# Kernel optimization log

Measured on AMD Instinct MI355X. Metric: run time of the kernel, lower is better.

Reference implementation:

```python
import jax, jax.numpy as jnp
import numpy as np

N_NODES = 100000


def setup_inputs() -> dict:
    key = jax.random.key(0)
    k1, k2, k3 = jax.random.split(key, 3)
    x = jax.random.normal(k1, (N_NODES, 64), dtype=jnp.float32)
    edge_index = jax.random.randint(k2, (2, 1250000), 0, N_NODES, dtype=jnp.int64)
    W = jax.random.normal(k3, (128, 64), dtype=jnp.float32) * (1.0 / np.sqrt(128.0))
    b = jnp.zeros((64,), dtype=jnp.float32)
    return {"x": x, "edge_index": edge_index, "W": W, "b": b}


def reference(x, edge_index, W, b):
    n = x.shape[0]
    row, col = edge_index[0], edge_index[1]
    # scatter-add neighbor features onto destination nodes
    neigh = jax.ops.segment_sum(x[row], col, num_segments=n)          # [n, d]
    count = jax.ops.segment_sum(jnp.ones_like(col, dtype=x.dtype), col, num_segments=n)
    count = jnp.where(count == 0, jnp.asarray(1.0, x.dtype), count)   # avoid div-by-zero
    neigh = neigh / count[:, None]                                    # mean aggregation
    x_aggr = jnp.concatenate([x, neigh], axis=-1)                     # [n, 2d]
    out = x_aggr @ W + b                                              # [n, out_dim]
    return jax.nn.relu(out)  # dropout=0.0 (eval) -> identity
```

## Files before the change

### kernel.cpp

```cpp
#include <hip/hip_runtime.h>

#define D 64
#define NPB 64
#define THREADS 512
#define CAP 64

typedef int v4i __attribute__((ext_vector_type(4)));
typedef short bf16x8 __attribute__((ext_vector_type(8)));
typedef float f32x4 __attribute__((ext_vector_type(4)));

__device__ __forceinline__ unsigned short f2bf(float f) {
  unsigned u = __float_as_uint(f);
  return (unsigned short)((u + 0x7FFFu + ((u >> 16) & 1u)) >> 16);
}
__device__ __forceinline__ float bf2f(unsigned short h) {
  return __uint_as_float(((unsigned)h) << 16);
}
__device__ __forceinline__ void bfsplit(float v, unsigned short& hi, unsigned short& lo) {
  unsigned u = __float_as_uint(v);
  hi = (unsigned short)(u >> 16);
  float r = v - __uint_as_float(u & 0xFFFF0000u);
  lo = f2bf(r);
}

__global__ __launch_bounds__(256) void prep0_kernel(
    const float* __restrict__ x, ushort* __restrict__ xh,
    int* __restrict__ cnt, const float* __restrict__ W,
    ushort* __restrict__ wth, ushort* __restrict__ wtl,
    int n, int total4) {
  int t = blockIdx.x * blockDim.x + threadIdx.x;
  int nth = gridDim.x * blockDim.x;
  for (int i = t; i < n; i += nth) cnt[i] = 0;
  for (int i = t; i < 2 * D * D; i += nth) {
    int nn = i >> 7, k = i & 127;
    float v = W[k * D + nn];
    unsigned short hi, lo;
    bfsplit(v, hi, lo);
    wth[i] = hi;
    wtl[i] = lo;
  }
  for (int i = t; i < total4; i += nth) {
    float4 v = ((const float4*)x)[i];
    ushort4 h;
    h.x = f2bf(v.x); h.y = f2bf(v.y); h.z = f2bf(v.z); h.w = f2bf(v.w);
    ((ushort4*)xh)[i] = h;
  }
}

__global__ __launch_bounds__(256) void fill_xcd_kernel(
    const int* __restrict__ ei, int* __restrict__ cnt,
    int* __restrict__ bucket, int e, int qpc) {
  const int myx = blockIdx.x & 7;
  const int chunk = blockIdx.x >> 3;
  const int quads = e >> 2;
  const v4i* row4 = (const v4i*)ei;
  const v4i* col4 = (const v4i*)(ei + e);
  int qend = chunk * qpc + qpc;
  if (qend > quads) qend = quads;
  for (int q = chunk * qpc + threadIdx.x; q < qend; q += 256) {
    v4i r = __builtin_nontemporal_load(&row4[q]);
    v4i c = __builtin_nontemporal_load(&col4[q]);
    if (((c.x >> 11) & 7) == myx) {
      int p = atomicAdd(&cnt[c.x], 1);
      if (p < CAP) bucket[(size_t)c.x * CAP + p] = r.x * D;
    }
    if (((c.y >> 11) & 7) == myx) {
      int p = atomicAdd(&cnt[c.y], 1);
      if (p < CAP) bucket[(size_t)c.y * CAP + p] = r.y * D;
    }
    if (((c.z >> 11) & 7) == myx) {
      int p = atomicAdd(&cnt[c.z], 1);
      if (p < CAP) bucket[(size_t)c.z * CAP + p] = r.z * D;
    }
    if (((c.w >> 11) & 7) == myx) {
      int p = atomicAdd(&cnt[c.w], 1);
      if (p < CAP) bucket[(size_t)c.w * CAP + p] = r.w * D;
    }
  }
}

__global__ __launch_bounds__(THREADS, 8) void fused_bf_kernel(
    const float* __restrict__ x, const ushort* __restrict__ xh,
    const int* __restrict__ cnt,
    const ushort* __restrict__ wth, const ushort* __restrict__ wtl,
    const float* __restrict__ b, float* __restrict__ out, int n) {
  __shared__ __align__(16) ushort xsh[NPB * 128];
  __shared__ __align__(16) ushort xsl[NPB * 128];

  const int lane = threadIdx.x & 63;
  const int wid  = threadIdx.x >> 6;
  const int base = blockIdx.x * NPB;
  const int* bucket = (const int*)out;
  const ushort* xpl = xh + lane;

  for (int m = 0; m < 8; ++m) {
    int nl = wid * 8 + m;
    int node = base + nl;
    int koff = nl * 128;
    int k0 = lane ^ ((nl & 7) << 3);
    if (node < n) {
      int dg = cnt[node];
      int dc = dg < CAP ? dg : CAP;
      int bk = bucket[(size_t)node * CAP + lane];
      float xown = x[(size_t)node * D + lane];
      float s0 = 0.f, s1 = 0.f, s2 = 0.f, s3 = 0.f;
      float s4 = 0.f, s5 = 0.f, s6 = 0.f, s7 = 0.f;
      int p = 0;
      for (; p + 8 <= dc; p += 8) {
        int a0 = __shfl(bk, p),     a1 = __shfl(bk, p + 1);
        int a2 = __shfl(bk, p + 2), a3 = __shfl(bk, p + 3);
        int a4 = __shfl(bk, p + 4), a5 = __shfl(bk, p + 5);
        int a6 = __shfl(bk, p + 6), a7 = __shfl(bk, p + 7);
        s0 += bf2f(xpl[a0]); s1 += bf2f(xpl[a1]);
        s2 += bf2f(xpl[a2]); s3 += bf2f(xpl[a3]);
        s4 += bf2f(xpl[a4]); s5 += bf2f(xpl[a5]);
        s6 += bf2f(xpl[a6]); s7 += bf2f(xpl[a7]);
      }
      for (; p + 4 <= dc; p += 4) {
        int a0 = __shfl(bk, p),     a1 = __shfl(bk, p + 1);
        int a2 = __shfl(bk, p + 2), a3 = __shfl(bk, p + 3);
        s0 += bf2f(xpl[a0]); s1 += bf2f(xpl[a1]);
        s2 += bf2f(xpl[a2]); s3 += bf2f(xpl[a3]);
      }
      for (; p < dc; ++p)
        s0 += bf2f(xpl[__shfl(bk, p)]);
      float sum = ((s0 + s1) + (s2 + s3)) + ((s4 + s5) + (s6 + s7));
      float inv = (dg > 0) ? (1.0f / (float)dg) : 0.0f;
      float mean = sum * inv;
      unsigned short h, l;
      bfsplit(xown, h, l);
      xsh[koff + k0] = h;       xsl[koff + k0] = l;
      bfsplit(mean, h, l);
      xsh[koff + 64 + k0] = h;  xsl[koff + 64 + k0] = l;
    } else {
      xsh[koff + k0] = 0;       xsl[koff + k0] = 0;
      xsh[koff + 64 + k0] = 0;  xsl[koff + 64 + k0] = 0;
    }
  }
  __syncthreads();

  const int mt   = wid >> 1;
  const int nb   = (wid & 1) * 32;
  const int lrow = lane & 15;
  const int kgrp = (lane >> 4) * 8;

  const int arow = mt * 16 + lrow;
  const int aswz = (arow & 7) << 3;
  const int abase = arow * 128;

  const ushort* wh0 = wth + (nb + lrow) * 128;
  const ushort* wh1 = wth + (nb + 16 + lrow) * 128;
  const ushort* wl0 = wtl + (nb + lrow) * 128;
  const ushort* wl1 = wtl + (nb + 16 + lrow) * 128;

  float bias0 = b[nb + lrow];
  float bias1 = b[nb + 16 + lrow];
  f32x4 acc0 = {bias0, bias0, bias0, bias0};
  f32x4 acc1 = {bias1, bias1, bias1, bias1};

#pragma unroll 2
  for (int ks = 0; ks < 4; ++ks) {
    int kb = ks * 32 + kgrp;
    int ke = abase + (kb ^ aswz);
    bf16x8 ah = *(const bf16x8*)&xsh[ke];
    bf16x8 al = *(const bf16x8*)&xsl[ke];
    bf16x8 w0h = *(const bf16x8*)(wh0 + kb);
    bf16x8 w1h = *(const bf16x8*)(wh1 + kb);
    acc0 = __builtin_amdgcn_mfma_f32_16x16x32_bf16(ah, w0h, acc0, 0, 0, 0);
    acc1 = __builtin_amdgcn_mfma_f32_16x16x32_bf16(ah, w1h, acc1, 0, 0, 0);
    acc0 = __builtin_amdgcn_mfma_f32_16x16x32_bf16(al, w0h, acc0, 0, 0, 0);
    acc1 = __builtin_amdgcn_mfma_f32_16x16x32_bf16(al, w1h, acc1, 0, 0, 0);
    bf16x8 w0l = *(const bf16x8*)(wl0 + kb);
    bf16x8 w1l = *(const bf16x8*)(wl1 + kb);
    acc0 = __builtin_amdgcn_mfma_f32_16x16x32_bf16(ah, w0l, acc0, 0, 0, 0);
    acc1 = __builtin_amdgcn_mfma_f32_16x16x32_bf16(ah, w1l, acc1, 0, 0, 0);
  }

  const int drow = (lane >> 4) * 4;
#pragma unroll
  for (int r = 0; r < 4; ++r) {
    int node = base + mt * 16 + drow + r;
    if (node < n) {
      out[(size_t)node * D + nb + lrow]      = fmaxf(acc0[r], 0.0f);
      out[(size_t)node * D + nb + 16 + lrow] = fmaxf(acc1[r], 0.0f);
    }
  }
}

__global__ __launch_bounds__(256) void fill_cap_kernel(
    const int* __restrict__ ei, int* __restrict__ cnt,
    int* __restrict__ bucket, int e) {
  int t = blockIdx.x * blockDim.x + threadIdx.x;
  if (t * 4 >= e) return;
  int4 r4 = ((const int4*)ei)[t];
  int4 c4 = ((const int4*)(ei + e))[t];
  int p0 = atomicAdd(&cnt[c4.x], 1);
  int p1 = atomicAdd(&cnt[c4.y], 1);
  int p2 = atomicAdd(&cnt[c4.z], 1);
  int p3 = atomicAdd(&cnt[c4.w], 1);
  if (p0 < CAP) bucket[(size_t)c4.x * CAP + p0] = r4.x;
  if (p1 < CAP) bucket[(size_t)c4.y * CAP + p1] = r4.y;
  if (p2 < CAP) bucket[(size_t)c4.z * CAP + p2] = r4.z;
  if (p3 < CAP) bucket[(size_t)c4.w * CAP + p3] = r4.w;
}

__global__ __launch_bounds__(THREADS, 8) void fused_cap_kernel(
    const float* __restrict__ x, const int* __restrict__ cnt,
    const float* __restrict__ W, const float* __restrict__ b,
    float* __restrict__ out, int n) {
  __shared__ __align__(16) float xs[NPB * 128];
  const int lane = threadIdx.x & 63;
  const int wid  = threadIdx.x >> 6;
  const int base = blockIdx.x * NPB;
  const int* bucket = (const int*)out;

  for (int m = 0; m < 8; ++m) {
    int nl = wid * 8 + m;
    int node = base + nl;
    if (node < n) {
      int dg = cnt[node];
      int dc = dg < CAP ? dg : CAP;
      int bk = bucket[(size_t)node * CAP + lane];
      float xown = x[(size_t)node * D + lane];
      float s0 = 0.f, s1 = 0.f, s2 = 0.f, s3 = 0.f;
      int p = 0;
      for (; p + 4 <= dc; p += 4) {
        int a0 = __shfl(bk, p),     a1 = __shfl(bk, p + 1);
        int a2 = __shfl(bk, p + 2), a3 = __shfl(bk, p + 3);
        s0 += x[(size_t)a0 * D + lane];
        s1 += x[(size_t)a1 * D + lane];
        s2 += x[(size_t)a2 * D + lane];
        s3 += x[(size_t)a3 * D + lane];
      }
      for (; p < dc; ++p)
        s0 += x[(size_t)__shfl(bk, p) * D + lane];
      float sum = (s0 + s1) + (s2 + s3);
      float inv = (dg > 0) ? (1.0f / (float)dg) : 0.0f;
      xs[nl * 128 + lane]      = xown;
      xs[nl * 128 + 64 + lane] = sum * inv;
    } else {
      xs[nl * 128 + lane]      = 0.0f;
      xs[nl * 128 + 64 + lane] = 0.0f;
    }
  }
  __syncthreads();

  const int col = lane;
  float bias = b[col];
  float acc[8];
#pragma unroll
  for (int m = 0; m < 8; ++m) acc[m] = bias;
  for (int k = 0; k < 128; k += 4) {
    float w0 = W[(k + 0) * 64 + col];
    float w1 = W[(k + 1) * 64 + col];
    float w2 = W[(k + 2) * 64 + col];
    float w3 = W[(k + 3) * 64 + col];
#pragma unroll
    for (int m = 0; m < 8; ++m) {
      int nl = wid + m * 8;
      float4 xv = *(const float4*)&xs[nl * 128 + k];
      acc[m] = fmaf(xv.x, w0, acc[m]);
      acc[m] = fmaf(xv.y, w1, acc[m]);
      acc[m] = fmaf(xv.z, w2, acc[m]);
      acc[m] = fmaf(xv.w, w3, acc[m]);
    }
  }
#pragma unroll
  for (int m = 0; m < 8; ++m) {
    int node = base + wid + m * 8;
    if (node < n)
      out[(size_t)node * D + col] = fmaxf(acc[m], 0.0f);
  }
}

extern "C" void kernel_launch(void* const* d_in, const int* in_sizes, int n_in,
                              void* d_out, int out_size, void* d_ws, size_t ws_size,
                              hipStream_t stream) {
  const float* x = (const float*)d_in[0];
  const int* ei = (const int*)d_in[1];
  const float* W = (const float*)d_in[2];
  const float* b = (const float*)d_in[3];
  float* out = (float*)d_out;

  int n = in_sizes[0] / D;
  int e = in_sizes[1] / 2;
  int nblocks = (n + NPB - 1) / NPB;

  size_t xh_bytes = (size_t)n * D * sizeof(ushort);
  size_t off = (xh_bytes + 255) & ~(size_t)255;
  size_t cnt_off = off;
  off += (((size_t)n * sizeof(int)) + 255) & ~(size_t)255;
  size_t wth_off = off;  off += 2 * D * D * sizeof(ushort);
  size_t wtl_off = off;  off += 2 * D * D * sizeof(ushort);
  size_t need = off + 256;

  if (ws_size >= need && (e & 3) == 0 && n <= (1 << 17)) {
    ushort* xh  = (ushort*)d_ws;
    int* cnt    = (int*)((char*)d_ws + cnt_off);
    ushort* wth = (ushort*)((char*)d_ws + wth_off);
    ushort* wtl = (ushort*)((char*)d_ws + wtl_off);

    int total4 = n * D / 4;
    prep0_kernel<<<2048, 256, 0, stream>>>(x, xh, cnt, W, wth, wtl, n, total4);

    int quads = e >> 2;
    int qpc = (quads + 255) / 256;
    fill_xcd_kernel<<<256 * 8, 256, 0, stream>>>(ei, cnt, (int*)d_out, e, qpc);

    fused_bf_kernel<<<nblocks, THREADS, 0, stream>>>(x, xh, cnt, wth, wtl, b, out, n);
  } else {
    int* cnt = (int*)d_ws;
    (void)hipMemsetAsync(cnt, 0, (size_t)n * sizeof(int), stream);
    int quads = e / 4;
    fill_cap_kernel<<<(quads + 255) / 256, 256, 0, stream>>>(ei, cnt, (int*)d_out, e);
    fused_cap_kernel<<<nblocks, THREADS, 0, stream>>>(x, cnt, W, b, out, n);
  }
}
```

Measured before the change: 205.8 us.

## Merge fill and prep kernels, use persistent atomic-tile fused kernel with prefetch

The edge bucketing fill and the x/W bf16 conversion now run in one launch, split by block index, so the conversion overlaps the atomic-heavy scatter. Zeroing of the counts moves to a memset that also clears a new tile counter. The fused aggregate+GEMM kernel becomes persistent: 1024 blocks take 64-node tiles from an atomic counter, prefetch the next node's degree, bucket row and own features, and use nontemporal loads and stores. The cost is an extra memset launch, a per-tile atomic, and extra barriers per tile.

```diff
diff --git a/kernel.cpp b/kernel.cpp
--- a/kernel.cpp
+++ b/kernel.cpp
@@ -4,6 +4,7 @@
 #define NPB 64
 #define THREADS 512
 #define CAP 64
+#define NFILL 2048
 
 typedef int v4i __attribute__((ext_vector_type(4)));
 typedef short bf16x8 __attribute__((ext_vector_type(8)));
@@ -23,58 +24,56 @@
   lo = f2bf(r);
 }
 
-__global__ __launch_bounds__(256) void prep0_kernel(
+__global__ __launch_bounds__(256) void fill_prep_kernel(
+    const int* __restrict__ ei, int* __restrict__ cnt,
+    int* __restrict__ bucket, int e, int qpc,
     const float* __restrict__ x, ushort* __restrict__ xh,
-    int* __restrict__ cnt, const float* __restrict__ W,
-    ushort* __restrict__ wth, ushort* __restrict__ wtl,
-    int n, int total4) {
-  int t = blockIdx.x * blockDim.x + threadIdx.x;
-  int nth = gridDim.x * blockDim.x;
-  for (int i = t; i < n; i += nth) cnt[i] = 0;
-  for (int i = t; i < 2 * D * D; i += nth) {
-    int nn = i >> 7, k = i & 127;
-    float v = W[k * D + nn];
-    unsigned short hi, lo;
-    bfsplit(v, hi, lo);
-    wth[i] = hi;
-    wtl[i] = lo;
-  }
-  for (int i = t; i < total4; i += nth) {
-    float4 v = ((const float4*)x)[i];
-    ushort4 h;
-    h.x = f2bf(v.x); h.y = f2bf(v.y); h.z = f2bf(v.z); h.w = f2bf(v.w);
-    ((ushort4*)xh)[i] = h;
-  }
-}
-
-__global__ __launch_bounds__(256) void fill_xcd_kernel(
-    const int* __restrict__ ei, int* __restrict__ cnt,
-    int* __restrict__ bucket, int e, int qpc) {
-  const int myx = blockIdx.x & 7;
-  const int chunk = blockIdx.x >> 3;
-  const int quads = e >> 2;
-  const v4i* row4 = (const v4i*)ei;
-  const v4i* col4 = (const v4i*)(ei + e);
-  int qend = chunk * qpc + qpc;
-  if (qend > quads) qend = quads;
-  for (int q = chunk * qpc + threadIdx.x; q < qend; q += 256) {
-    v4i r = __builtin_nontemporal_load(&row4[q]);
-    v4i c = __builtin_nontemporal_load(&col4[q]);
-    if (((c.x >> 11) & 7) == myx) {
-      int p = atomicAdd(&cnt[c.x], 1);
-      if (p < CAP) bucket[(size_t)c.x * CAP + p] = r.x * D;
-    }
-    if (((c.y >> 11) & 7) == myx) {
-      int p = atomicAdd(&cnt[c.y], 1);
-      if (p < CAP) bucket[(size_t)c.y * CAP + p] = r.y * D;
-    }
-    if (((c.z >> 11) & 7) == myx) {
-      int p = atomicAdd(&cnt[c.z], 1);
-      if (p < CAP) bucket[(size_t)c.z * CAP + p] = r.z * D;
-    }
-    if (((c.w >> 11) & 7) == myx) {
-      int p = atomicAdd(&cnt[c.w], 1);
-      if (p < CAP) bucket[(size_t)c.w * CAP + p] = r.w * D;
+    const float* __restrict__ W, ushort* __restrict__ wth,
+    ushort* __restrict__ wtl, int n, int total4) {
+  if (blockIdx.x < NFILL) {
+    const int myx = blockIdx.x & 7;
+    const int chunk = blockIdx.x >> 3;
+    const int quads = e >> 2;
+    const v4i* row4 = (const v4i*)ei;
+    const v4i* col4 = (const v4i*)(ei + e);
+    int qend = chunk * qpc + qpc;
+    if (qend > quads) qend = quads;
+    for (int q = chunk * qpc + threadIdx.x; q < qend; q += 256) {
+      v4i r = __builtin_nontemporal_load(&row4[q]);
+      v4i c = __builtin_nontemporal_load(&col4[q]);
+      if (((c.x >> 11) & 7) == myx) {
+        int p = atomicAdd(&cnt[c.x], 1);
+        if (p < CAP) bucket[(size_t)c.x * CAP + p] = r.x * D;
+      }
+      if (((c.y >> 11) & 7) == myx) {
+        int p = atomicAdd(&cnt[c.y], 1);
+        if (p < CAP) bucket[(size_t)c.y * CAP + p] = r.y * D;
+      }
+      if (((c.z >> 11) & 7) == myx) {
+        int p = atomicAdd(&cnt[c.z], 1);
+        if (p < CAP) bucket[(size_t)c.z * CAP + p] = r.z * D;
+      }
+      if (((c.w >> 11) & 7) == myx) {
+        int p = atomicAdd(&cnt[c.w], 1);
+        if (p < CAP) bucket[(size_t)c.w * CAP + p] = r.w * D;
+      }
+    }
+  } else {
+    int t = (blockIdx.x - NFILL) * 256 + threadIdx.x;
+    int nth = (gridDim.x - NFILL) * 256;
+    for (int i = t; i < 2 * D * D; i += nth) {
+      int nn = i >> 7, k = i & 127;
+      float v = W[k * D + nn];
+      unsigned short hi, lo;
+      bfsplit(v, hi, lo);
+      wth[i] = hi;
+      wtl[i] = lo;
+    }
+    for (int i = t; i < total4; i += nth) {
+      float4 v = ((const float4*)x)[i];
+      ushort4 h;
+      h.x = f2bf(v.x); h.y = f2bf(v.y); h.z = f2bf(v.z); h.w = f2bf(v.w);
+      ((ushort4*)xh)[i] = h;
     }
   }
 }
@@ -83,107 +82,135 @@
     const float* __restrict__ x, const ushort* __restrict__ xh,
     const int* __restrict__ cnt,
     const ushort* __restrict__ wth, const ushort* __restrict__ wtl,
-    const float* __restrict__ b, float* __restrict__ out, int n) {
+    const float* __restrict__ b, float* __restrict__ out,
+    int n, int ntiles, int* __restrict__ tctr) {
   __shared__ __align__(16) ushort xsh[NPB * 128];
   __shared__ __align__(16) ushort xsl[NPB * 128];
+  __shared__ int s_tile;
 
   const int lane = threadIdx.x & 63;
   const int wid  = threadIdx.x >> 6;
-  const int base = blockIdx.x * NPB;
   const int* bucket = (const int*)out;
   const ushort* xpl = xh + lane;
-
-  for (int m = 0; m < 8; ++m) {
-    int nl = wid * 8 + m;
-    int node = base + nl;
-    int koff = nl * 128;
-    int k0 = lane ^ ((nl & 7) << 3);
-    if (node < n) {
-      int dg = cnt[node];
-      int dc = dg < CAP ? dg : CAP;
-      int bk = bucket[(size_t)node * CAP + lane];
-      float xown = x[(size_t)node * D + lane];
-      float s0 = 0.f, s1 = 0.f, s2 = 0.f, s3 = 0.f;
-      float s4 = 0.f, s5 = 0.f, s6 = 0.f, s7 = 0.f;
-      int p = 0;
-      for (; p + 8 <= dc; p += 8) {
-        int a0 = __shfl(bk, p),     a1 = __shfl(bk, p + 1);
-        int a2 = __shfl(bk, p + 2), a3 = __shfl(bk, p + 3);
-        int a4 = __shfl(bk, p + 4), a5 = __shfl(bk, p + 5);
-        int a6 = __shfl(bk, p + 6), a7 = __shfl(bk, p + 7);
-        s0 += bf2f(xpl[a0]); s1 += bf2f(xpl[a1]);
-        s2 += bf2f(xpl[a2]); s3 += bf2f(xpl[a3]);
-        s4 += bf2f(xpl[a4]); s5 += bf2f(xpl[a5]);
-        s6 += bf2f(xpl[a6]); s7 += bf2f(xpl[a7]);
-      }
-      for (; p + 4 <= dc; p += 4) {
-        int a0 = __shfl(bk, p),     a1 = __shfl(bk, p + 1);
-        int a2 = __shfl(bk, p + 2), a3 = __shfl(bk, p + 3);
-        s0 += bf2f(xpl[a0]); s1 += bf2f(xpl[a1]);
-        s2 += bf2f(xpl[a2]); s3 += bf2f(xpl[a3]);
-      }
-      for (; p < dc; ++p)
-        s0 += bf2f(xpl[__shfl(bk, p)]);
-      float sum = ((s0 + s1) + (s2 + s3)) + ((s4 + s5) + (s6 + s7));
-      float inv = (dg > 0) ? (1.0f / (float)dg) : 0.0f;
-      float mean = sum * inv;
-      unsigned short h, l;
-      bfsplit(xown, h, l);
-      xsh[koff + k0] = h;       xsl[koff + k0] = l;
-      bfsplit(mean, h, l);
-      xsh[koff + 64 + k0] = h;  xsl[koff + 64 + k0] = l;
-    } else {
-      xsh[koff + k0] = 0;       xsl[koff + k0] = 0;
-      xsh[koff + 64 + k0] = 0;  xsl[koff + 64 + k0] = 0;
-    }
-  }
-  __syncthreads();
 
   const int mt   = wid >> 1;
   const int nb   = (wid & 1) * 32;
   const int lrow = lane & 15;
   const int kgrp = (lane >> 4) * 8;
-
   const int arow = mt * 16 + lrow;
   const int aswz = (arow & 7) << 3;
   const int abase = arow * 128;
-
   const ushort* wh0 = wth + (nb + lrow) * 128;
   const ushort* wh1 = wth + (nb + 16 + lrow) * 128;
   const ushort* wl0 = wtl + (nb + lrow) * 128;
   const ushort* wl1 = wtl + (nb + 16 + lrow) * 128;
-
-  float bias0 = b[nb + lrow];
-  float bias1 = b[nb + 16 + lrow];
-  f32x4 acc0 = {bias0, bias0, bias0, bias0};
-  f32x4 acc1 = {bias1, bias1, bias1, bias1};
-
+  const float bias0 = b[nb + lrow];
+  const float bias1 = b[nb + 16 + lrow];
+  const int drow = (lane >> 4) * 4;
+
+  for (;;) {
+    if (threadIdx.x == 0) s_tile = atomicAdd(tctr, 1);
+    __syncthreads();
+    const int tile = s_tile;
+    if (tile >= ntiles) break;
+    const int base = tile * NPB;
+
+    {
+      int node0 = base + wid * 8;
+      int dgN = 0, bkN = 0;
+      float xoN = 0.f;
+      if (node0 < n) {
+        dgN = cnt[node0];
+        bkN = __builtin_nontemporal_load(&bucket[(size_t)node0 * CAP + lane]);
+        xoN = __builtin_nontemporal_load(&x[(size_t)node0 * D + lane]);
+      }
+      for (int m = 0; m < 8; ++m) {
+        int nl = wid * 8 + m;
+        int node = base + nl;
+        int dg = dgN, bk = bkN;
+        float xown = xoN;
+        if (m < 7) {
+          int nq = node + 1;
+          if (nq < n) {
+            dgN = cnt[nq];
+            bkN = __builtin_nontemporal_load(&bucket[(size_t)nq * CAP + lane]);
+            xoN = __builtin_nontemporal_load(&x[(size_t)nq * D + lane]);
+          } else {
+            dgN = 0; bkN = 0; xoN = 0.f;
+          }
+        }
+        int koff = nl * 128;
+        int k0 = lane ^ ((nl & 7) << 3);
+        if (node < n) {
+          int dc = dg < CAP ? dg : CAP;
+          float s0 = 0.f, s1 = 0.f, s2 = 0.f, s3 = 0.f;
+          float s4 = 0.f, s5 = 0.f, s6 = 0.f, s7 = 0.f;
+          int p = 0;
+          for (; p + 8 <= dc; p += 8) {
+            int a0 = __shfl(bk, p),     a1 = __shfl(bk, p + 1);
+            int a2 = __shfl(bk, p + 2), a3 = __shfl(bk, p + 3);
+            int a4 = __shfl(bk, p + 4), a5 = __shfl(bk, p + 5);
+            int a6 = __shfl(bk, p + 6), a7 = __shfl(bk, p + 7);
+            s0 += bf2f(xpl[a0]); s1 += bf2f(xpl[a1]);
+            s2 += bf2f(xpl[a2]); s3 += bf2f(xpl[a3]);
+            s4 += bf2f(xpl[a4]); s5 += bf2f(xpl[a5]);
+            s6 += bf2f(xpl[a6]); s7 += bf2f(xpl[a7]);
+          }
+          for (; p + 4 <= dc; p += 4) {
+            int a0 = __shfl(bk, p),     a1 = __shfl(bk, p + 1);
+            int a2 = __shfl(bk, p + 2), a3 = __shfl(bk, p + 3);
+            s0 += bf2f(xpl[a0]); s1 += bf2f(xpl[a1]);
+            s2 += bf2f(xpl[a2]); s3 += bf2f(xpl[a3]);
+          }
+          for (; p < dc; ++p)
+            s0 += bf2f(xpl[__shfl(bk, p)]);
+          float sum = ((s0 + s1) + (s2 + s3)) + ((s4 + s5) + (s6 + s7));
+          float inv = (dg > 0) ? (1.0f / (float)dg) : 0.0f;
+          float mean = sum * inv;
+          unsigned short h, l;
+          bfsplit(xown, h, l);
+          xsh[koff + k0] = h;       xsl[koff + k0] = l;
+          bfsplit(mean, h, l);
+          xsh[koff + 64 + k0] = h;  xsl[koff + 64 + k0] = l;
+        } else {
+          xsh[koff + k0] = 0;       xsl[koff + k0] = 0;
+          xsh[koff + 64 + k0] = 0;  xsl[koff + 64 + k0] = 0;
+        }
+      }
+    }
+    __syncthreads();
+
+    f32x4 acc0 = {bias0, bias0, bias0, bias0};
+    f32x4 acc1 = {bias1, bias1, bias1, bias1};
 #pragma unroll 2
-  for (int ks = 0; ks < 4; ++ks) {
-    int kb = ks * 32 + kgrp;
-    int ke = abase + (kb ^ aswz);
-    bf16x8 ah = *(const bf16x8*)&xsh[ke];
-    bf16x8 al = *(const bf16x8*)&xsl[ke];
-    bf16x8 w0h = *(const bf16x8*)(wh0 + kb);
-    bf16x8 w1h = *(const bf16x8*)(wh1 + kb);
-    acc0 = __builtin_amdgcn_mfma_f32_16x16x32_bf16(ah, w0h, acc0, 0, 0, 0);
-    acc1 = __builtin_amdgcn_mfma_f32_16x16x32_bf16(ah, w1h, acc1, 0, 0, 0);
-    acc0 = __builtin_amdgcn_mfma_f32_16x16x32_bf16(al, w0h, acc0, 0, 0, 0);
-    acc1 = __builtin_amdgcn_mfma_f32_16x16x32_bf16(al, w1h, acc1, 0, 0, 0);
-    bf16x8 w0l = *(const bf16x8*)(wl0 + kb);
-    bf16x8 w1l = *(const bf16x8*)(wl1 + kb);
-    acc0 = __builtin_amdgcn_mfma_f32_16x16x32_bf16(ah, w0l, acc0, 0, 0, 0);
-    acc1 = __builtin_amdgcn_mfma_f32_16x16x32_bf16(ah, w1l, acc1, 0, 0, 0);
-  }
-
-  const int drow = (lane >> 4) * 4;
+    for (int ks = 0; ks < 4; ++ks) {
+      int kb = ks * 32 + kgrp;
+      int ke = abase + (kb ^ aswz);
+      bf16x8 ah = *(const bf16x8*)&xsh[ke];
+      bf16x8 al = *(const bf16x8*)&xsl[ke];
+      bf16x8 w0h = *(const bf16x8*)(wh0 + kb);
+      bf16x8 w1h = *(const bf16x8*)(wh1 + kb);
+      acc0 = __builtin_amdgcn_mfma_f32_16x16x32_bf16(ah, w0h, acc0, 0, 0, 0);
+      acc1 = __builtin_amdgcn_mfma_f32_16x16x32_bf16(ah, w1h, acc1, 0, 0, 0);
+      acc0 = __builtin_amdgcn_mfma_f32_16x16x32_bf16(al, w0h, acc0, 0, 0, 0);
+      acc1 = __builtin_amdgcn_mfma_f32_16x16x32_bf16(al, w1h, acc1, 0, 0, 0);
+      bf16x8 w0l = *(const bf16x8*)(wl0 + kb);
+      bf16x8 w1l = *(const bf16x8*)(wl1 + kb);
+      acc0 = __builtin_amdgcn_mfma_f32_16x16x32_bf16(ah, w0l, acc0, 0, 0, 0);
+      acc1 = __builtin_amdgcn_mfma_f32_16x16x32_bf16(ah, w1l, acc1, 0, 0, 0);
+    }
+
 #pragma unroll
-  for (int r = 0; r < 4; ++r) {
-    int node = base + mt * 16 + drow + r;
-    if (node < n) {
-      out[(size_t)node * D + nb + lrow]      = fmaxf(acc0[r], 0.0f);
-      out[(size_t)node * D + nb + 16 + lrow] = fmaxf(acc1[r], 0.0f);
-    }
+    for (int r = 0; r < 4; ++r) {
+      int node = base + mt * 16 + drow + r;
+      if (node < n) {
+        __builtin_nontemporal_store(fmaxf(acc0[r], 0.0f),
+                                    &out[(size_t)node * D + nb + lrow]);
+        __builtin_nontemporal_store(fmaxf(acc1[r], 0.0f),
+                                    &out[(size_t)node * D + nb + 16 + lrow]);
+      }
+    }
+    __syncthreads();
   }
 }
 
@@ -284,35 +311,38 @@
 
   int n = in_sizes[0] / D;
   int e = in_sizes[1] / 2;
-  int nblocks = (n + NPB - 1) / NPB;
+  int ntiles = (n + NPB - 1) / NPB;
 
   size_t xh_bytes = (size_t)n * D * sizeof(ushort);
-  size_t off = (xh_bytes + 255) & ~(size_t)255;
-  size_t cnt_off = off;
-  off += (((size_t)n * sizeof(int)) + 255) & ~(size_t)255;
-  size_t wth_off = off;  off += 2 * D * D * sizeof(ushort);
-  size_t wtl_off = off;  off += 2 * D * D * sizeof(ushort);
-  size_t need = off + 256;
+  size_t cnt_off  = (xh_bytes + 255) & ~(size_t)255;
+  size_t tctr_off = (cnt_off + (size_t)n * sizeof(int) + 255) & ~(size_t)255;
+  size_t wth_off  = tctr_off + 256;
+  size_t wtl_off  = wth_off + 2 * D * D * sizeof(ushort);
+  size_t need     = wtl_off + 2 * D * D * sizeof(ushort) + 256;
 
   if (ws_size >= need && (e & 3) == 0 && n <= (1 << 17)) {
     ushort* xh  = (ushort*)d_ws;
     int* cnt    = (int*)((char*)d_ws + cnt_off);
+    int* tctr   = (int*)((char*)d_ws + tctr_off);
     ushort* wth = (ushort*)((char*)d_ws + wth_off);
     ushort* wtl = (ushort*)((char*)d_ws + wtl_off);
 
+    (void)hipMemsetAsync((char*)d_ws + cnt_off, 0,
+                         tctr_off + 256 - cnt_off, stream);
+
     int total4 = n * D / 4;
-    prep0_kernel<<<2048, 256, 0, stream>>>(x, xh, cnt, W, wth, wtl, n, total4);
-
     int quads = e >> 2;
     int qpc = (quads + 255) / 256;
-    fill_xcd_kernel<<<256 * 8, 256, 0, stream>>>(ei, cnt, (int*)d_out, e, qpc);
-
-    fused_bf_kernel<<<nblocks, THREADS, 0, stream>>>(x, xh, cnt, wth, wtl, b, out, n);
+    fill_prep_kernel<<<NFILL + 256, 256, 0, stream>>>(
+        ei, cnt, (int*)d_out, e, qpc, x, xh, W, wth, wtl, n, total4);
+
+    fused_bf_kernel<<<1024, THREADS, 0, stream>>>(
+        x, xh, cnt, wth, wtl, b, out, n, ntiles, tctr);
   } else {
     int* cnt = (int*)d_ws;
     (void)hipMemsetAsync(cnt, 0, (size_t)n * sizeof(int), stream);
     int quads = e / 4;
     fill_cap_kernel<<<(quads + 255) / 256, 256, 0, stream>>>(ei, cnt, (int*)d_out, e);
-    fused_cap_kernel<<<nblocks, THREADS, 0, stream>>>(x, cnt, W, b, out, n);
-  }
-}
+    fused_cap_kernel<<<ntiles, THREADS, 0, stream>>>(x, cnt, W, b, out, n);
+  }
+}
```

New measurement: 222.9 us. +8.3%, slower.

## Merge edge bucketing and bf16 conversion into one kernel with block specialization

Applied to the files above, without the earlier changes.

The separate prep and fill kernels become a single launch. The first 1792 blocks bucket edges by destination, and the remaining 256 blocks convert x and W to bf16 at the same time. Count zeroing moves to a hipMemsetAsync. This removes one kernel boundary and lets the memory-bound conversion overlap the atomic-heavy fill, but it adds a memset launch and gives the fill fewer blocks.

```diff
diff --git a/kernel.cpp b/kernel.cpp
--- a/kernel.cpp
+++ b/kernel.cpp
@@ -4,6 +4,8 @@
 #define NPB 64
 #define THREADS 512
 #define CAP 64
+#define NFILLB 1792
+#define NCONVB 256
 
 typedef int v4i __attribute__((ext_vector_type(4)));
 typedef short bf16x8 __attribute__((ext_vector_type(8)));
@@ -23,58 +25,56 @@
   lo = f2bf(r);
 }
 
-__global__ __launch_bounds__(256) void prep0_kernel(
+__global__ __launch_bounds__(256, 8) void fill_prep_kernel(
+    const int* __restrict__ ei, int* __restrict__ cnt,
+    int* __restrict__ bucket, int e, int qpc,
     const float* __restrict__ x, ushort* __restrict__ xh,
-    int* __restrict__ cnt, const float* __restrict__ W,
-    ushort* __restrict__ wth, ushort* __restrict__ wtl,
-    int n, int total4) {
-  int t = blockIdx.x * blockDim.x + threadIdx.x;
-  int nth = gridDim.x * blockDim.x;
-  for (int i = t; i < n; i += nth) cnt[i] = 0;
-  for (int i = t; i < 2 * D * D; i += nth) {
-    int nn = i >> 7, k = i & 127;
-    float v = W[k * D + nn];
-    unsigned short hi, lo;
-    bfsplit(v, hi, lo);
-    wth[i] = hi;
-    wtl[i] = lo;
-  }
-  for (int i = t; i < total4; i += nth) {
-    float4 v = ((const float4*)x)[i];
-    ushort4 h;
-    h.x = f2bf(v.x); h.y = f2bf(v.y); h.z = f2bf(v.z); h.w = f2bf(v.w);
-    ((ushort4*)xh)[i] = h;
-  }
-}
-
-__global__ __launch_bounds__(256) void fill_xcd_kernel(
-    const int* __restrict__ ei, int* __restrict__ cnt,
-    int* __restrict__ bucket, int e, int qpc) {
-  const int myx = blockIdx.x & 7;
-  const int chunk = blockIdx.x >> 3;
-  const int quads = e >> 2;
-  const v4i* row4 = (const v4i*)ei;
-  const v4i* col4 = (const v4i*)(ei + e);
-  int qend = chunk * qpc + qpc;
-  if (qend > quads) qend = quads;
-  for (int q = chunk * qpc + threadIdx.x; q < qend; q += 256) {
-    v4i r = __builtin_nontemporal_load(&row4[q]);
-    v4i c = __builtin_nontemporal_load(&col4[q]);
-    if (((c.x >> 11) & 7) == myx) {
-      int p = atomicAdd(&cnt[c.x], 1);
-      if (p < CAP) bucket[(size_t)c.x * CAP + p] = r.x * D;
-    }
-    if (((c.y >> 11) & 7) == myx) {
-      int p = atomicAdd(&cnt[c.y], 1);
-      if (p < CAP) bucket[(size_t)c.y * CAP + p] = r.y * D;
-    }
-    if (((c.z >> 11) & 7) == myx) {
-      int p = atomicAdd(&cnt[c.z], 1);
-      if (p < CAP) bucket[(size_t)c.z * CAP + p] = r.z * D;
-    }
-    if (((c.w >> 11) & 7) == myx) {
-      int p = atomicAdd(&cnt[c.w], 1);
-      if (p < CAP) bucket[(size_t)c.w * CAP + p] = r.w * D;
+    const float* __restrict__ W, ushort* __restrict__ wth,
+    ushort* __restrict__ wtl, int n, int total4) {
+  if (blockIdx.x < NFILLB) {
+    const int myx = blockIdx.x & 7;
+    const int chunk = blockIdx.x >> 3;
+    const int quads = e >> 2;
+    const v4i* row4 = (const v4i*)ei;
+    const v4i* col4 = (const v4i*)(ei + e);
+    int qend = chunk * qpc + qpc;
+    if (qend > quads) qend = quads;
+    for (int q = chunk * qpc + threadIdx.x; q < qend; q += 256) {
+      v4i r = __builtin_nontemporal_load(&row4[q]);
+      v4i c = __builtin_nontemporal_load(&col4[q]);
+      if (((c.x >> 11) & 7) == myx) {
+        int p = atomicAdd(&cnt[c.x], 1);
+        if (p < CAP) bucket[(size_t)c.x * CAP + p] = r.x * D;
+      }
+      if (((c.y >> 11) & 7) == myx) {
+        int p = atomicAdd(&cnt[c.y], 1);
+        if (p < CAP) bucket[(size_t)c.y * CAP + p] = r.y * D;
+      }
+      if (((c.z >> 11) & 7) == myx) {
+        int p = atomicAdd(&cnt[c.z], 1);
+        if (p < CAP) bucket[(size_t)c.z * CAP + p] = r.z * D;
+      }
+      if (((c.w >> 11) & 7) == myx) {
+        int p = atomicAdd(&cnt[c.w], 1);
+        if (p < CAP) bucket[(size_t)c.w * CAP + p] = r.w * D;
+      }
+    }
+  } else {
+    int t = (blockIdx.x - NFILLB) * 256 + threadIdx.x;
+    int nth = NCONVB * 256;
+    for (int i = t; i < 2 * D * D; i += nth) {
+      int nn = i >> 7, k = i & 127;
+      float v = W[k * D + nn];
+      unsigned short hi, lo;
+      bfsplit(v, hi, lo);
+      wth[i] = hi;
+      wtl[i] = lo;
+    }
+    for (int i = t; i < total4; i += nth) {
+      float4 v = ((const float4*)x)[i];
+      ushort4 h;
+      h.x = f2bf(v.x); h.y = f2bf(v.y); h.z = f2bf(v.z); h.w = f2bf(v.w);
+      ((ushort4*)xh)[i] = h;
     }
   }
 }
@@ -287,27 +287,29 @@
   int nblocks = (n + NPB - 1) / NPB;
 
   size_t xh_bytes = (size_t)n * D * sizeof(ushort);
-  size_t off = (xh_bytes + 255) & ~(size_t)255;
-  size_t cnt_off = off;
-  off += (((size_t)n * sizeof(int)) + 255) & ~(size_t)255;
-  size_t wth_off = off;  off += 2 * D * D * sizeof(ushort);
-  size_t wtl_off = off;  off += 2 * D * D * sizeof(ushort);
-  size_t need = off + 256;
+  size_t cnt_off  = (xh_bytes + 255) & ~(size_t)255;
+  size_t wth_off  = (cnt_off + (size_t)n * sizeof(int) + 255) & ~(size_t)255;
+  size_t wtl_off  = wth_off + 2 * D * D * sizeof(ushort);
+  size_t need     = wtl_off + 2 * D * D * sizeof(ushort) + 256;
 
   if (ws_size >= need && (e & 3) == 0 && n <= (1 << 17)) {
-    ushort* xh  = (ushort*)d_ws;
-    int* cnt    = (int*)((char*)d_ws + cnt_off);
-    ushort* wth = (ushort*)((char*)d_ws + wth_off);
-    ushort* wtl = (ushort*)((char*)d_ws + wtl_off);
+    ushort* xh   = (ushort*)d_ws;
+    int* cnt     = (int*)((char*)d_ws + cnt_off);
+    ushort* wth  = (ushort*)((char*)d_ws + wth_off);
+    ushort* wtl  = (ushort*)((char*)d_ws + wtl_off);
+
+    (void)hipMemsetAsync(cnt, 0, (size_t)n * sizeof(int), stream);
 
     int total4 = n * D / 4;
-    prep0_kernel<<<2048, 256, 0, stream>>>(x, xh, cnt, W, wth, wtl, n, total4);
-
     int quads = e >> 2;
-    int qpc = (quads + 255) / 256;
-    fill_xcd_kernel<<<256 * 8, 256, 0, stream>>>(ei, cnt, (int*)d_out, e, qpc);
-
-    fused_bf_kernel<<<nblocks, THREADS, 0, stream>>>(x, xh, cnt, wth, wtl, b, out, n);
+    int chunks = NFILLB / 8;
+    int qpc = (quads + chunks - 1) / chunks;
+
+    fill_prep_kernel<<<NFILLB + NCONVB, 256, 0, stream>>>(
+        ei, cnt, (int*)d_out, e, qpc, x, xh, W, wth, wtl, n, total4);
+
+    fused_bf_kernel<<<nblocks, THREADS, 0, stream>>>(
+        x, xh, cnt, wth, wtl, b, out, n);
   } else {
     int* cnt = (int*)d_ws;
     (void)hipMemsetAsync(cnt, 0, (size_t)n * sizeof(int), stream);
```

Result: no change. 202.1 us (-1.8%).
